# Kernel tuning notes

Hardware: AMD Instinct MI355X
Metric: run time of the kernel (lower is better)

## Reference

```python
import jax, jax.numpy as jnp
import numpy as np

B, GEO_CH, SEM_CH, H, W = 8, 256, 256, 64, 64
HS, WS = 32, 32  # semantic branch spatial size
EPS_ATTN = 1e-6
EPS_GN = 1e-5


def _phi(x):
    return jax.nn.elu(x) + 1.0


def setup_inputs() -> dict:
    key = jax.random.key(0)
    ks = jax.random.split(key, 8)
    f_geo = jax.random.normal(ks[0], (B, GEO_CH, H, W), dtype=jnp.float32)
    f_sem = jax.random.normal(ks[1], (B, SEM_CH, HS, WS), dtype=jnp.float32)
    s = 0.02
    Wq = jax.random.normal(ks[2], (SEM_CH, GEO_CH), dtype=jnp.float32) * s
    Wk = jax.random.normal(ks[3], (SEM_CH, SEM_CH), dtype=jnp.float32) * s
    Wv = jax.random.normal(ks[4], (SEM_CH, SEM_CH), dtype=jnp.float32) * s
    Wo = jax.random.normal(ks[5], (GEO_CH, SEM_CH), dtype=jnp.float32) * s
    bq = jnp.zeros((SEM_CH,), jnp.float32)
    bk = jnp.zeros((SEM_CH,), jnp.float32)
    bv = jnp.zeros((SEM_CH,), jnp.float32)
    bo = jnp.zeros((GEO_CH,), jnp.float32)
    gn_w = jnp.ones((GEO_CH,), jnp.float32)
    gn_b = jnp.zeros((GEO_CH,), jnp.float32)
    return {"f_geo": f_geo, "f_sem": f_sem, "Wq": Wq, "bq": bq, "Wk": Wk,
            "bk": bk, "Wv": Wv, "bv": bv, "Wo": Wo, "bo": bo,
            "gn_w": gn_w, "gn_b": gn_b}


def _conv1x1(x, Wm, b):
    # x: [B,Cin,H,W], Wm: [Cout,Cin] -> [B,Cout,H,W]
    return jnp.einsum('oc,bchw->bohw', Wm, x) + b[None, :, None, None]


def reference(f_geo, f_sem, Wq, bq, Wk, bk, Wv, bv, Wo, bo, gn_w, gn_b):
    b, cg, h, w = f_geo.shape
    n = h * w
    # bilinear resize, half-pixel centers == torch align_corners=False
    f_sem_r = jax.image.resize(f_sem, (b, f_sem.shape[1], h, w), method='bilinear')
    Q = _phi(_conv1x1(f_geo, Wq, bq)).reshape(b, -1, n)      # [B,Cs,N]
    K = _phi(_conv1x1(f_sem_r, Wk, bk)).reshape(b, -1, n)    # [B,Cs,N]
    V = _conv1x1(f_sem_r, Wv, bv).reshape(b, -1, n)          # [B,Cs,N]
    KV = jnp.einsum('bcn,bdn->bcd', K, V)                    # [B,Cs,Cs]
    QKV = jnp.einsum('bcn,bcd->bnd', Q, KV)                  # [B,N,Cs]
    K_sum = K.sum(axis=-1)                                   # [B,Cs]
    norm = jnp.einsum('bcn,bc->bn', Q, K_sum)[..., None] + EPS_ATTN  # [B,N,1]
    out = (QKV / norm).transpose(0, 2, 1).reshape(b, -1, h, w)
    y = f_geo + _conv1x1(out, Wo, bo)
    # GroupNorm(1, geo_ch): normalize over (C,H,W) per sample, per-channel affine
    mu = y.mean(axis=(1, 2, 3), keepdims=True)
    var = y.var(axis=(1, 2, 3), keepdims=True)
    yn = (y - mu) * jax.lax.rsqrt(var + EPS_GN)
    return yn * gn_w[None, :, None, None] + gn_b[None, :, None, None]
```

## Files before the change

kernel.cpp:

```cpp
#include <hip/hip_runtime.h>
#include <hip/hip_bf16.h>


#define B_ 8
#define C_ 256
#define H_ 64
#define W_ 64
#define N_ 4096
#define NS_ 1024
#define PIT 40
#define LDSZ (4 * 128 * PIT)
#define KVCH 16

typedef unsigned short u16;
using bf16x8 = __attribute__((ext_vector_type(8))) short;
using f32x4 = __attribute__((ext_vector_type(4))) float;

__device__ inline u16 f2bf(float f) {
  unsigned u = __builtin_bit_cast(unsigned, f);
  unsigned r = (u + 0x7fffu + ((u >> 16) & 1u)) >> 16;
  return (u16)r;
}
__device__ inline float bf2f(u16 x) {
  return __builtin_bit_cast(float, ((unsigned)x) << 16);
}

__device__ inline void gemm128_nt(const u16* __restrict__ At, const u16* __restrict__ Bt,
                                  int lda, int ldb, int k0, int k1,
                                  u16* __restrict__ lds, f32x4 acc[4][4])
{
  const int t = threadIdx.x;
  const int lane = t & 63;
  const int wave = t >> 6;
  const int wr = wave >> 1, wc = wave & 1;
  const int lr = lane & 15, lg = lane >> 4;
  const int sr = t >> 2, skv = t & 3;
  const size_t aoff = (size_t)sr * lda + skv * 8;
  const size_t aoff2 = (size_t)(sr + 64) * lda + skv * 8;
  const size_t boff = (size_t)sr * ldb + skv * 8;
  const size_t boff2 = (size_t)(sr + 64) * ldb + skv * 8;
  const int woff = sr * PIT + skv * 8;
  u16* A0 = lds;
  u16* B0 = lds + 128 * PIT;
  u16* A1 = lds + 2 * 128 * PIT;
  u16* B1 = lds + 3 * 128 * PIT;

  {
    uint4 a0 = *reinterpret_cast<const uint4*>(&At[aoff + k0]);
    uint4 a1 = *reinterpret_cast<const uint4*>(&At[aoff2 + k0]);
    uint4 b0 = *reinterpret_cast<const uint4*>(&Bt[boff + k0]);
    uint4 b1 = *reinterpret_cast<const uint4*>(&Bt[boff2 + k0]);
    *reinterpret_cast<uint4*>(&A0[woff]) = a0;
    *reinterpret_cast<uint4*>(&A0[woff + 64 * PIT]) = a1;
    *reinterpret_cast<uint4*>(&B0[woff]) = b0;
    *reinterpret_cast<uint4*>(&B0[woff + 64 * PIT]) = b1;
  }
  __syncthreads();
  int cur = 0;
  for (int k = k0; k < k1; k += 32) {
    uint4 na0, na1, nb0, nb1;
    const bool more = (k + 32) < k1;
    if (more) {
      na0 = *reinterpret_cast<const uint4*>(&At[aoff + k + 32]);
      na1 = *reinterpret_cast<const uint4*>(&At[aoff2 + k + 32]);
      nb0 = *reinterpret_cast<const uint4*>(&Bt[boff + k + 32]);
      nb1 = *reinterpret_cast<const uint4*>(&Bt[boff2 + k + 32]);
    }
    const u16* Ar = cur ? A1 : A0;
    const u16* Br = cur ? B1 : B0;
    const u16* ab = &Ar[(wr * 64 + lr) * PIT + lg * 8];
    const u16* bb = &Br[(wc * 64 + lr) * PIT + lg * 8];
    bf16x8 af[4], bfr[4];
#pragma unroll
    for (int i = 0; i < 4; ++i) af[i] = *reinterpret_cast<const bf16x8*>(ab + i * 16 * PIT);
#pragma unroll
    for (int i = 0; i < 4; ++i) bfr[i] = *reinterpret_cast<const bf16x8*>(bb + i * 16 * PIT);
#pragma unroll
    for (int m = 0; m < 4; ++m)
#pragma unroll
      for (int n = 0; n < 4; ++n)
        acc[m][n] = __builtin_amdgcn_mfma_f32_16x16x32_bf16(af[m], bfr[n], acc[m][n], 0, 0, 0);
    if (more) {
      u16* Aw = cur ? A0 : A1;
      u16* Bw = cur ? B0 : B1;
      *reinterpret_cast<uint4*>(&Aw[woff]) = na0;
      *reinterpret_cast<uint4*>(&Aw[woff + 64 * PIT]) = na1;
      *reinterpret_cast<uint4*>(&Bw[woff]) = nb0;
      *reinterpret_cast<uint4*>(&Bw[woff + 64 * PIT]) = nb1;
    }
    __syncthreads();
    cur ^= 1;
  }
}

__device__ inline void zero_acc(f32x4 acc[4][4]) {
#pragma unroll
  for (int m = 0; m < 4; ++m)
#pragma unroll
    for (int n = 0; n < 4; ++n)
#pragma unroll
      for (int r = 0; r < 4; ++r) acc[m][n][r] = 0.f;
}

__global__ __launch_bounds__(256) void k_transpose_cast(const float* __restrict__ in,
                                                        u16* __restrict__ out, int rows, int cols)
{
  __shared__ float tile[32][33];
  int b = blockIdx.z;
  const float* src = in + (size_t)b * rows * cols;
  u16* dst = out + (size_t)b * rows * cols;
  int c0 = blockIdx.x * 32, r0 = blockIdx.y * 32;
  int tx = threadIdx.x & 31, ty = threadIdx.x >> 5;
#pragma unroll
  for (int i = 0; i < 32; i += 8)
    tile[ty + i][tx] = src[(size_t)(r0 + ty + i) * cols + (c0 + tx)];
  __syncthreads();
#pragma unroll
  for (int i = 0; i < 32; i += 8)
    dst[(size_t)(c0 + ty + i) * rows + (r0 + tx)] = f2bf(tile[tx][ty + i]);
}

__global__ __launch_bounds__(256) void k_cast4(const float* __restrict__ w0, const float* __restrict__ w1,
                                               const float* __restrict__ w2, const float* __restrict__ w3,
                                               u16* o0, u16* o1, u16* o2, u16* o3,
                                               float* __restrict__ stats, float* __restrict__ normv)
{
  int i = blockIdx.x * 256 + threadIdx.x;
  o0[i] = f2bf(w0[i]); o1[i] = f2bf(w1[i]); o2[i] = f2bf(w2[i]); o3[i] = f2bf(w3[i]);
  if (i < 16) stats[i] = 0.f;
  if (i < B_ * N_) normv[i] = 1e-6f;
}

__global__ __launch_bounds__(256) void k_semconv(const u16* __restrict__ fsemT,
                                                 const u16* __restrict__ Wk, const u16* __restrict__ Wv,
                                                 const float* __restrict__ bk, const float* __restrict__ bv,
                                                 u16* __restrict__ Kpre, u16* __restrict__ Vpre)
{
  __shared__ u16 lds[LDSZ];
  int b = blockIdx.z >> 1, sel = blockIdx.z & 1;
  int m0 = blockIdx.y * 128, n0 = blockIdx.x * 128;
  const u16* A = (sel ? Wv : Wk) + (size_t)m0 * C_;
  const u16* Bm = fsemT + (size_t)b * NS_ * C_ + (size_t)n0 * C_;
  const float* bias = sel ? bv : bk;
  u16* out = (sel ? Vpre : Kpre) + (size_t)b * C_ * NS_;
  f32x4 acc[4][4];
  zero_acc(acc);
  gemm128_nt(A, Bm, C_, C_, 0, C_, lds, acc);
  int lane = threadIdx.x & 63, wave = threadIdx.x >> 6;
  int wr = wave >> 1, wc = wave & 1, lr = lane & 15, lg = lane >> 4;
#pragma unroll
  for (int m = 0; m < 4; ++m)
#pragma unroll
    for (int r = 0; r < 4; ++r) {
      int row = m0 + wr * 64 + m * 16 + lg * 4 + r;
      float bi = bias[row];
#pragma unroll
      for (int n = 0; n < 4; ++n) {
        int col = n0 + wc * 64 + n * 16 + lr;
        out[(size_t)row * NS_ + col] = f2bf(acc[m][n][r] + bi);
      }
    }
}

__global__ __launch_bounds__(256) void k_resize(const u16* __restrict__ Kpre, const u16* __restrict__ Vpre,
                                                u16* __restrict__ Kbf, u16* __restrict__ Vbf,
                                                float* __restrict__ Ksum)
{
  int sel = blockIdx.y;
  const u16* src = (sel ? Vpre : Kpre) + (size_t)blockIdx.x * NS_;
  u16* dst = (sel ? Vbf : Kbf) + (size_t)blockIdx.x * N_;
  float s = 0.f;
  for (int i = threadIdx.x; i < N_; i += 256) {
    int yy = i >> 6, xx = i & 63;
    int yh = yy >> 1, xh = xx >> 1;
    int ys0, ys1, xs0, xs1; float wy0, wy1, wx0, wx1;
    if (yy & 1) { ys0 = yh; ys1 = yh < 31 ? yh + 1 : 31; wy0 = 0.75f; wy1 = 0.25f; }
    else        { ys0 = yh > 0 ? yh - 1 : 0; ys1 = yh;   wy0 = 0.25f; wy1 = 0.75f; }
    if (xx & 1) { xs0 = xh; xs1 = xh < 31 ? xh + 1 : 31; wx0 = 0.75f; wx1 = 0.25f; }
    else        { xs0 = xh > 0 ? xh - 1 : 0; xs1 = xh;   wx0 = 0.25f; wx1 = 0.75f; }
    float r0 = wx0 * bf2f(src[ys0 * 32 + xs0]) + wx1 * bf2f(src[ys0 * 32 + xs1]);
    float r1 = wx0 * bf2f(src[ys1 * 32 + xs0]) + wx1 * bf2f(src[ys1 * 32 + xs1]);
    float v = wy0 * r0 + wy1 * r1;
    if (!sel) { v = v > 0.f ? v + 1.f : __expf(v); s += v; }
    dst[i] = f2bf(v);
  }
  if (!sel) {
    __shared__ float red[256];
    red[threadIdx.x] = s; __syncthreads();
    for (int off = 128; off > 0; off >>= 1) {
      if (threadIdx.x < off) red[threadIdx.x] += red[threadIdx.x + off];
      __syncthreads();
    }
    if (threadIdx.x == 0) Ksum[blockIdx.x] = red[0];
  }
}

__global__ __launch_bounds__(256) void k_kv(const u16* __restrict__ Kbf, const u16* __restrict__ Vbf,
                                            float* __restrict__ KVpart)
{
  __shared__ u16 lds[LDSZ];
  int tn = blockIdx.x, tm = blockIdx.y;
  int b = blockIdx.z >> 4, ch = blockIdx.z & 15;
  const int kspan = N_ / KVCH;
  const u16* A = Kbf + (size_t)b * C_ * N_ + (size_t)tm * 128 * N_;
  const u16* Bm = Vbf + (size_t)b * C_ * N_ + (size_t)tn * 128 * N_;
  f32x4 acc[4][4];
  zero_acc(acc);
  gemm128_nt(A, Bm, N_, N_, ch * kspan, ch * kspan + kspan, lds, acc);
  float* out = KVpart + ((size_t)(b * KVCH + ch) * 4 + tm * 2 + tn) * (128 * 128);
  int lane = threadIdx.x & 63, wave = threadIdx.x >> 6;
  int wr = wave >> 1, wc = wave & 1, lr = lane & 15, lg = lane >> 4;
#pragma unroll
  for (int m = 0; m < 4; ++m)
#pragma unroll
    for (int r = 0; r < 4; ++r)
#pragma unroll
      for (int n = 0; n < 4; ++n)
        out[(size_t)(wr * 64 + m * 16 + lg * 4 + r) * 128 + wc * 64 + n * 16 + lr] = acc[m][n][r];
}

__global__ __launch_bounds__(256) void k_kvred(const float* __restrict__ KVpart, u16* __restrict__ KVbf)
{
  int idx = blockIdx.x * 256 + threadIdx.x;
  int b = idx >> 16, cd = idx & 65535;
  int c = cd >> 8, d = cd & 255;
  int tile = (c >> 7) * 2 + (d >> 7);
  int loc = (c & 127) * 128 + (d & 127);
  float s = 0.f;
#pragma unroll
  for (int ch = 0; ch < KVCH; ++ch)
    s += KVpart[((size_t)(b * KVCH + ch) * 4 + tile) * 16384 + loc];
  KVbf[idx] = f2bf(s);
}

__global__ __launch_bounds__(256) void k_mgemm(const u16* __restrict__ Wo, const u16* __restrict__ KVbf,
                                               u16* __restrict__ Mbf)
{
  __shared__ u16 lds[LDSZ];
  int tn = blockIdx.x, tm = blockIdx.y, b = blockIdx.z;
  const u16* A = Wo + (size_t)tm * 128 * C_;
  const u16* Bm = KVbf + (size_t)b * C_ * C_ + (size_t)tn * 128 * C_;
  f32x4 acc[4][4];
  zero_acc(acc);
  gemm128_nt(A, Bm, C_, C_, 0, C_, lds, acc);
  u16* out = Mbf + (size_t)b * C_ * C_;
  int lane = threadIdx.x & 63, wave = threadIdx.x >> 6;
  int wr = wave >> 1, wc = wave & 1, lr = lane & 15, lg = lane >> 4;
#pragma unroll
  for (int m = 0; m < 4; ++m)
#pragma unroll
    for (int r = 0; r < 4; ++r)
#pragma unroll
      for (int n = 0; n < 4; ++n)
        out[(size_t)(tm * 128 + wr * 64 + m * 16 + lg * 4 + r) * C_ +
            tn * 128 + wc * 64 + n * 16 + lr] = f2bf(acc[m][n][r]);
}

__global__ __launch_bounds__(256) void k_qgemm(const u16* __restrict__ fgeoT, const u16* __restrict__ Wq,
                                               const float* __restrict__ bq, const float* __restrict__ Ksum,
                                               u16* __restrict__ Qt, float* __restrict__ normv)
{
  __shared__ u16 lds[LDSZ];
  int tc = blockIdx.x, tn = blockIdx.y, b = blockIdx.z;
  const u16* A = fgeoT + (size_t)b * N_ * C_ + (size_t)tn * 128 * C_;
  const u16* Bm = Wq + (size_t)tc * 128 * C_;
  f32x4 acc[4][4];
  zero_acc(acc);
  gemm128_nt(A, Bm, C_, C_, 0, C_, lds, acc);
  u16* out = Qt + (size_t)b * N_ * C_;
  int lane = threadIdx.x & 63, wave = threadIdx.x >> 6;
  int wr = wave >> 1, wc = wave & 1, lr = lane & 15, lg = lane >> 4;
  float bqv[4], ksv[4];
#pragma unroll
  for (int n = 0; n < 4; ++n) {
    int c = tc * 128 + wc * 64 + n * 16 + lr;
    bqv[n] = bq[c];
    ksv[n] = Ksum[b * C_ + c];
  }
  float pn[4][4];
#pragma unroll
  for (int m = 0; m < 4; ++m)
#pragma unroll
    for (int r = 0; r < 4; ++r) {
      int row = tn * 128 + wr * 64 + m * 16 + lg * 4 + r;
      float p = 0.f;
#pragma unroll
      for (int n = 0; n < 4; ++n) {
        float v = acc[m][n][r] + bqv[n];
        v = v > 0.f ? v + 1.f : __expf(v);
        out[(size_t)row * C_ + tc * 128 + wc * 64 + n * 16 + lr] = f2bf(v);
        p += v * ksv[n];
      }
      pn[m][r] = p;
    }
#pragma unroll
  for (int m = 0; m < 4; ++m)
#pragma unroll
    for (int r = 0; r < 4; ++r) {
      float p = pn[m][r];
      p += __shfl_xor(p, 1); p += __shfl_xor(p, 2);
      p += __shfl_xor(p, 4); p += __shfl_xor(p, 8);
      pn[m][r] = p;
    }
  if (lr == 0) {
    float* nb = normv + (size_t)b * N_;
#pragma unroll
    for (int m = 0; m < 4; ++m)
#pragma unroll
      for (int r = 0; r < 4; ++r) {
        int row = tn * 128 + wr * 64 + m * 16 + lg * 4 + r;
        atomicAdd(&nb[row], pn[m][r]);
      }
  }
}

__global__ __launch_bounds__(256) void k_final(const u16* __restrict__ Mbf, const u16* __restrict__ Qt,
                                               const float* __restrict__ fgeo, const float* __restrict__ bo,
                                               const float* __restrict__ normv,
                                               float* __restrict__ y, float* __restrict__ stats)
{
  __shared__ u16 lds[LDSZ];
  int tn = blockIdx.x, tm = blockIdx.y, b = blockIdx.z;
  const u16* A = Mbf + (size_t)b * C_ * C_ + (size_t)tm * 128 * C_;
  const u16* Bm = Qt + (size_t)b * N_ * C_ + (size_t)tn * 128 * C_;
  f32x4 acc[4][4];
  zero_acc(acc);
  gemm128_nt(A, Bm, C_, C_, 0, C_, lds, acc);
  int lane = threadIdx.x & 63, wave = threadIdx.x >> 6;
  int wr = wave >> 1, wc = wave & 1, lr = lane & 15, lg = lane >> 4;
  int m0 = tm * 128, n0 = tn * 128;
  const float* nrm = normv + (size_t)b * N_;
  float nv[4];
#pragma unroll
  for (int n = 0; n < 4; ++n) nv[n] = nrm[n0 + wc * 64 + n * 16 + lr];
  const float* fg = fgeo + (size_t)b * C_ * N_;
  float* yb = y + (size_t)b * C_ * N_;
  float ssum = 0.f, ssq = 0.f;
#pragma unroll
  for (int m = 0; m < 4; ++m)
#pragma unroll
    for (int r = 0; r < 4; ++r) {
      int row = m0 + wr * 64 + m * 16 + lg * 4 + r;
      float bov = bo[row];
#pragma unroll
      for (int n = 0; n < 4; ++n) {
        int col = n0 + wc * 64 + n * 16 + lr;
        float val = fg[(size_t)row * N_ + col] + bov + acc[m][n][r] / nv[n];
        yb[(size_t)row * N_ + col] = val;
        ssum += val; ssq += val * val;
      }
    }
#pragma unroll
  for (int off = 1; off < 64; off <<= 1) {
    ssum += __shfl_xor(ssum, off);
    ssq += __shfl_xor(ssq, off);
  }
  if (lane == 0) {
    atomicAdd(&stats[b * 2], ssum);
    atomicAdd(&stats[b * 2 + 1], ssq);
  }
}

__global__ __launch_bounds__(256) void k_gn(float* __restrict__ y, const float* __restrict__ stats,
                                            const float* __restrict__ gnw, const float* __restrict__ gnb)
{
  int idx = blockIdx.x * 256 + threadIdx.x;
  int elem = idx * 8;
  int b = elem >> 20;
  int o = (elem >> 12) & 255;
  const float cnt = (float)C_ * (float)N_;
  float mu = stats[b * 2] / cnt;
  float var = stats[b * 2 + 1] / cnt - mu * mu;
  float rs = rsqrtf(var + 1e-5f);
  float sc = gnw[o] * rs;
  float sh = gnb[o] - mu * sc;
  float4* p = reinterpret_cast<float4*>(y) + idx * 2;
  float4 v0 = p[0], v1 = p[1];
  v0.x = v0.x * sc + sh; v0.y = v0.y * sc + sh; v0.z = v0.z * sc + sh; v0.w = v0.w * sc + sh;
  v1.x = v1.x * sc + sh; v1.y = v1.y * sc + sh; v1.z = v1.z * sc + sh; v1.w = v1.w * sc + sh;
  p[0] = v0; p[1] = v1;
}

extern "C" void kernel_launch(void* const* d_in, const int* in_sizes, int n_in,
                              void* d_out, int out_size, void* d_ws, size_t ws_size,
                              hipStream_t stream)
{
  const float* f_geo = (const float*)d_in[0];
  const float* f_sem = (const float*)d_in[1];
  const float* Wq = (const float*)d_in[2];
  const float* bq = (const float*)d_in[3];
  const float* Wk = (const float*)d_in[4];
  const float* bk = (const float*)d_in[5];
  const float* Wv = (const float*)d_in[6];
  const float* bv = (const float*)d_in[7];
  const float* Wo = (const float*)d_in[8];
  const float* bo = (const float*)d_in[9];
  const float* gnw = (const float*)d_in[10];
  const float* gnb = (const float*)d_in[11];
  float* y = (float*)d_out;

  char* w = (char*)d_ws;
  auto alloc = [&](size_t bytes) { char* p = w; w += (bytes + 255) & ~(size_t)255; return p; };
  u16* fsemT = (u16*)alloc((size_t)B_ * NS_ * C_ * 2);
  u16* fgeoT = (u16*)alloc((size_t)B_ * N_ * C_ * 2);
  u16* Wqb = (u16*)alloc(65536 * 2);
  u16* Wkb = (u16*)alloc(65536 * 2);
  u16* Wvb = (u16*)alloc(65536 * 2);
  u16* Wob = (u16*)alloc(65536 * 2);
  u16* Kpre = (u16*)alloc((size_t)B_ * C_ * NS_ * 2);
  u16* Vpre = (u16*)alloc((size_t)B_ * C_ * NS_ * 2);
  u16* Kbf = (u16*)alloc((size_t)B_ * C_ * N_ * 2);
  u16* Vbf = (u16*)alloc((size_t)B_ * C_ * N_ * 2);
  float* Ksum = (float*)alloc((size_t)B_ * C_ * 4);
  float* KVpart = (float*)alloc((size_t)B_ * KVCH * 4 * 16384 * 4);
  u16* KVbf = (u16*)alloc((size_t)B_ * C_ * C_ * 2);
  u16* Mbf = (u16*)alloc((size_t)B_ * C_ * C_ * 2);
  u16* Qt = (u16*)alloc((size_t)B_ * N_ * C_ * 2);
  float* normv = (float*)alloc((size_t)B_ * N_ * 4);
  float* stats = (float*)alloc(256);

  k_transpose_cast<<<dim3(NS_ / 32, C_ / 32, B_), 256, 0, stream>>>(f_sem, fsemT, C_, NS_);
  k_transpose_cast<<<dim3(N_ / 32, C_ / 32, B_), 256, 0, stream>>>(f_geo, fgeoT, C_, N_);
  k_cast4<<<dim3(256), 256, 0, stream>>>(Wq, Wk, Wv, Wo, Wqb, Wkb, Wvb, Wob, stats, normv);
  k_semconv<<<dim3(8, 2, 16), 256, 0, stream>>>(fsemT, Wkb, Wvb, bk, bv, Kpre, Vpre);
  k_resize<<<dim3(B_ * C_, 2), 256, 0, stream>>>(Kpre, Vpre, Kbf, Vbf, Ksum);
  k_kv<<<dim3(2, 2, B_ * KVCH), 256, 0, stream>>>(Kbf, Vbf, KVpart);
  k_kvred<<<dim3(2048), 256, 0, stream>>>(KVpart, KVbf);
  k_mgemm<<<dim3(2, 2, B_), 256, 0, stream>>>(Wob, KVbf, Mbf);
  k_qgemm<<<dim3(2, 32, B_), 256, 0, stream>>>(fgeoT, Wqb, bq, Ksum, Qt, normv);
  k_final<<<dim3(32, 2, B_), 256, 0, stream>>>(Mbf, Qt, f_geo, bo, normv, y, stats);
  k_gn<<<dim3(B_ * C_ * N_ / 8 / 256), 256, 0, stream>>>(y, stats, gnw, gnb);
}
```

Measured before the change: 270.1 us.

## Use direct global-to-LDS loads in GEMM and stage epilogues through LDS

The shared GEMM mainloop now uses global_load_lds to copy tiles straight into unpadded LDS, dropping the register round-trip and the software double buffer. It relies on two barriers per k-step instead. All GEMM epilogues stage accumulators through an LDS buffer in two halves so each thread writes coalesced float4/ushort4 rows, and the q-GEMM norm reduction is reorganized around that. The risks are LDS bank conflicts from the unpadded 32-wide layout and less overlap of loads with MFMA work now that there is no prefetch.

```diff
diff --git a/kernel.cpp b/kernel.cpp
--- a/kernel.cpp
+++ b/kernel.cpp
@@ -4,12 +4,8 @@
 
 #define B_ 8
 #define C_ 256
-#define H_ 64
-#define W_ 64
 #define N_ 4096
 #define NS_ 1024
-#define PIT 40
-#define LDSZ (4 * 128 * PIT)
 #define KVCH 16
 
 typedef unsigned short u16;
@@ -25,71 +21,49 @@
   return __builtin_bit_cast(float, ((unsigned)x) << 16);
 }
 
+__device__ __forceinline__ void gl_lds16(const u16* g, u16* l) {
+  __builtin_amdgcn_global_load_lds((const __attribute__((address_space(1))) void*)g,
+                                   (__attribute__((address_space(3))) void*)l, 16, 0, 0);
+}
+
 __device__ inline void gemm128_nt(const u16* __restrict__ At, const u16* __restrict__ Bt,
                                   int lda, int ldb, int k0, int k1,
                                   u16* __restrict__ lds, f32x4 acc[4][4])
 {
   const int t = threadIdx.x;
-  const int lane = t & 63;
-  const int wave = t >> 6;
+  const int lane = t & 63, wave = t >> 6;
   const int wr = wave >> 1, wc = wave & 1;
   const int lr = lane & 15, lg = lane >> 4;
-  const int sr = t >> 2, skv = t & 3;
-  const size_t aoff = (size_t)sr * lda + skv * 8;
-  const size_t aoff2 = (size_t)(sr + 64) * lda + skv * 8;
-  const size_t boff = (size_t)sr * ldb + skv * 8;
-  const size_t boff2 = (size_t)(sr + 64) * ldb + skv * 8;
-  const int woff = sr * PIT + skv * 8;
-  u16* A0 = lds;
-  u16* B0 = lds + 128 * PIT;
-  u16* A1 = lds + 2 * 128 * PIT;
-  u16* B1 = lds + 3 * 128 * PIT;
-
-  {
-    uint4 a0 = *reinterpret_cast<const uint4*>(&At[aoff + k0]);
-    uint4 a1 = *reinterpret_cast<const uint4*>(&At[aoff2 + k0]);
-    uint4 b0 = *reinterpret_cast<const uint4*>(&Bt[boff + k0]);
-    uint4 b1 = *reinterpret_cast<const uint4*>(&Bt[boff2 + k0]);
-    *reinterpret_cast<uint4*>(&A0[woff]) = a0;
-    *reinterpret_cast<uint4*>(&A0[woff + 64 * PIT]) = a1;
-    *reinterpret_cast<uint4*>(&B0[woff]) = b0;
-    *reinterpret_cast<uint4*>(&B0[woff + 64 * PIT]) = b1;
-  }
-  __syncthreads();
-  int cur = 0;
+  const int sr = t >> 2, skv = (t & 3) * 8;
+  u16* Ab = lds;
+  u16* Bb = lds + 128 * 32;
+  const u16* gA0 = At + (size_t)sr * lda + skv;
+  const u16* gA1 = At + (size_t)(sr + 64) * lda + skv;
+  const u16* gB0 = Bt + (size_t)sr * ldb + skv;
+  const u16* gB1 = Bt + (size_t)(sr + 64) * ldb + skv;
+  u16* dA0 = Ab + wave * 512;
+  u16* dA1 = Ab + 2048 + wave * 512;
+  u16* dB0 = Bb + wave * 512;
+  u16* dB1 = Bb + 2048 + wave * 512;
+  const u16* ap = Ab + (wr * 64 + lr) * 32 + lg * 8;
+  const u16* bp = Bb + (wc * 64 + lr) * 32 + lg * 8;
   for (int k = k0; k < k1; k += 32) {
-    uint4 na0, na1, nb0, nb1;
-    const bool more = (k + 32) < k1;
-    if (more) {
-      na0 = *reinterpret_cast<const uint4*>(&At[aoff + k + 32]);
-      na1 = *reinterpret_cast<const uint4*>(&At[aoff2 + k + 32]);
-      nb0 = *reinterpret_cast<const uint4*>(&Bt[boff + k + 32]);
-      nb1 = *reinterpret_cast<const uint4*>(&Bt[boff2 + k + 32]);
-    }
-    const u16* Ar = cur ? A1 : A0;
-    const u16* Br = cur ? B1 : B0;
-    const u16* ab = &Ar[(wr * 64 + lr) * PIT + lg * 8];
-    const u16* bb = &Br[(wc * 64 + lr) * PIT + lg * 8];
+    gl_lds16(gA0 + k, dA0);
+    gl_lds16(gA1 + k, dA1);
+    gl_lds16(gB0 + k, dB0);
+    gl_lds16(gB1 + k, dB1);
+    __syncthreads();
     bf16x8 af[4], bfr[4];
 #pragma unroll
-    for (int i = 0; i < 4; ++i) af[i] = *reinterpret_cast<const bf16x8*>(ab + i * 16 * PIT);
-#pragma unroll
-    for (int i = 0; i < 4; ++i) bfr[i] = *reinterpret_cast<const bf16x8*>(bb + i * 16 * PIT);
+    for (int i = 0; i < 4; ++i) af[i] = *reinterpret_cast<const bf16x8*>(ap + i * 16 * 32);
+#pragma unroll
+    for (int i = 0; i < 4; ++i) bfr[i] = *reinterpret_cast<const bf16x8*>(bp + i * 16 * 32);
 #pragma unroll
     for (int m = 0; m < 4; ++m)
 #pragma unroll
       for (int n = 0; n < 4; ++n)
         acc[m][n] = __builtin_amdgcn_mfma_f32_16x16x32_bf16(af[m], bfr[n], acc[m][n], 0, 0, 0);
-    if (more) {
-      u16* Aw = cur ? A0 : A1;
-      u16* Bw = cur ? B0 : B1;
-      *reinterpret_cast<uint4*>(&Aw[woff]) = na0;
-      *reinterpret_cast<uint4*>(&Aw[woff + 64 * PIT]) = na1;
-      *reinterpret_cast<uint4*>(&Bw[woff]) = nb0;
-      *reinterpret_cast<uint4*>(&Bw[woff + 64 * PIT]) = nb1;
-    }
-    __syncthreads();
-    cur ^= 1;
+    __syncthreads();
   }
 }
 
@@ -100,6 +74,20 @@
     for (int n = 0; n < 4; ++n)
 #pragma unroll
       for (int r = 0; r < 4; ++r) acc[m][n][r] = 0.f;
+}
+
+__device__ inline void ep_stage_half(const f32x4 acc[4][4], float* eplds, int h,
+                                     int wr, int wc, int lr, int lg)
+{
+  if (wr == h) {
+#pragma unroll
+    for (int m = 0; m < 4; ++m)
+#pragma unroll
+      for (int n = 0; n < 4; ++n)
+#pragma unroll
+        for (int r = 0; r < 4; ++r)
+          eplds[(m * 16 + lg * 4 + r) * 132 + wc * 64 + n * 16 + lr] = acc[m][n][r];
+  }
 }
 
 __global__ __launch_bounds__(256) void k_transpose_cast(const float* __restrict__ in,
@@ -136,7 +124,8 @@
                                                  const float* __restrict__ bk, const float* __restrict__ bv,
                                                  u16* __restrict__ Kpre, u16* __restrict__ Vpre)
 {
-  __shared__ u16 lds[LDSZ];
+  __shared__ u16 glds[2 * 128 * 32];
+  __shared__ float eplds[64 * 132];
   int b = blockIdx.z >> 1, sel = blockIdx.z & 1;
   int m0 = blockIdx.y * 128, n0 = blockIdx.x * 128;
   const u16* A = (sel ? Wv : Wk) + (size_t)m0 * C_;
@@ -145,21 +134,24 @@
   u16* out = (sel ? Vpre : Kpre) + (size_t)b * C_ * NS_;
   f32x4 acc[4][4];
   zero_acc(acc);
-  gemm128_nt(A, Bm, C_, C_, 0, C_, lds, acc);
-  int lane = threadIdx.x & 63, wave = threadIdx.x >> 6;
+  gemm128_nt(A, Bm, C_, C_, 0, C_, glds, acc);
+  int t = threadIdx.x, lane = t & 63, wave = t >> 6;
   int wr = wave >> 1, wc = wave & 1, lr = lane & 15, lg = lane >> 4;
-#pragma unroll
-  for (int m = 0; m < 4; ++m)
-#pragma unroll
-    for (int r = 0; r < 4; ++r) {
-      int row = m0 + wr * 64 + m * 16 + lg * 4 + r;
+  for (int h = 0; h < 2; ++h) {
+    __syncthreads();
+    ep_stage_half(acc, eplds, h, wr, wc, lr, lg);
+    __syncthreads();
+#pragma unroll
+    for (int it = 0; it < 8; ++it) {
+      int rloc = it * 8 + (t >> 5), cloc = (t & 31) * 4;
+      int row = m0 + h * 64 + rloc;
+      float4 a = *(const float4*)&eplds[rloc * 132 + cloc];
       float bi = bias[row];
-#pragma unroll
-      for (int n = 0; n < 4; ++n) {
-        int col = n0 + wc * 64 + n * 16 + lr;
-        out[(size_t)row * NS_ + col] = f2bf(acc[m][n][r] + bi);
-      }
-    }
+      ushort4 o;
+      o.x = f2bf(a.x + bi); o.y = f2bf(a.y + bi); o.z = f2bf(a.z + bi); o.w = f2bf(a.w + bi);
+      *(ushort4*)&out[(size_t)row * NS_ + n0 + cloc] = o;
+    }
+  }
 }
 
 __global__ __launch_bounds__(256) void k_resize(const u16* __restrict__ Kpre, const u16* __restrict__ Vpre,
@@ -198,7 +190,8 @@
 __global__ __launch_bounds__(256) void k_kv(const u16* __restrict__ Kbf, const u16* __restrict__ Vbf,
                                             float* __restrict__ KVpart)
 {
-  __shared__ u16 lds[LDSZ];
+  __shared__ u16 glds[2 * 128 * 32];
+  __shared__ float eplds[64 * 132];
   int tn = blockIdx.x, tm = blockIdx.y;
   int b = blockIdx.z >> 4, ch = blockIdx.z & 15;
   const int kspan = N_ / KVCH;
@@ -206,17 +199,21 @@
   const u16* Bm = Vbf + (size_t)b * C_ * N_ + (size_t)tn * 128 * N_;
   f32x4 acc[4][4];
   zero_acc(acc);
-  gemm128_nt(A, Bm, N_, N_, ch * kspan, ch * kspan + kspan, lds, acc);
+  gemm128_nt(A, Bm, N_, N_, ch * kspan, ch * kspan + kspan, glds, acc);
   float* out = KVpart + ((size_t)(b * KVCH + ch) * 4 + tm * 2 + tn) * (128 * 128);
-  int lane = threadIdx.x & 63, wave = threadIdx.x >> 6;
+  int t = threadIdx.x, lane = t & 63, wave = t >> 6;
   int wr = wave >> 1, wc = wave & 1, lr = lane & 15, lg = lane >> 4;
-#pragma unroll
-  for (int m = 0; m < 4; ++m)
-#pragma unroll
-    for (int r = 0; r < 4; ++r)
-#pragma unroll
-      for (int n = 0; n < 4; ++n)
-        out[(size_t)(wr * 64 + m * 16 + lg * 4 + r) * 128 + wc * 64 + n * 16 + lr] = acc[m][n][r];
+  for (int h = 0; h < 2; ++h) {
+    __syncthreads();
+    ep_stage_half(acc, eplds, h, wr, wc, lr, lg);
+    __syncthreads();
+#pragma unroll
+    for (int it = 0; it < 8; ++it) {
+      int rloc = it * 8 + (t >> 5), cloc = (t & 31) * 4;
+      float4 a = *(const float4*)&eplds[rloc * 132 + cloc];
+      *(float4*)&out[(size_t)(h * 64 + rloc) * 128 + cloc] = a;
+    }
+  }
 }
 
 __global__ __launch_bounds__(256) void k_kvred(const float* __restrict__ KVpart, u16* __restrict__ KVbf)
@@ -236,81 +233,73 @@
 __global__ __launch_bounds__(256) void k_mgemm(const u16* __restrict__ Wo, const u16* __restrict__ KVbf,
                                                u16* __restrict__ Mbf)
 {
-  __shared__ u16 lds[LDSZ];
+  __shared__ u16 glds[2 * 128 * 32];
+  __shared__ float eplds[64 * 132];
   int tn = blockIdx.x, tm = blockIdx.y, b = blockIdx.z;
   const u16* A = Wo + (size_t)tm * 128 * C_;
   const u16* Bm = KVbf + (size_t)b * C_ * C_ + (size_t)tn * 128 * C_;
   f32x4 acc[4][4];
   zero_acc(acc);
-  gemm128_nt(A, Bm, C_, C_, 0, C_, lds, acc);
+  gemm128_nt(A, Bm, C_, C_, 0, C_, glds, acc);
   u16* out = Mbf + (size_t)b * C_ * C_;
-  int lane = threadIdx.x & 63, wave = threadIdx.x >> 6;
+  int t = threadIdx.x, lane = t & 63, wave = t >> 6;
   int wr = wave >> 1, wc = wave & 1, lr = lane & 15, lg = lane >> 4;
-#pragma unroll
-  for (int m = 0; m < 4; ++m)
-#pragma unroll
-    for (int r = 0; r < 4; ++r)
-#pragma unroll
-      for (int n = 0; n < 4; ++n)
-        out[(size_t)(tm * 128 + wr * 64 + m * 16 + lg * 4 + r) * C_ +
-            tn * 128 + wc * 64 + n * 16 + lr] = f2bf(acc[m][n][r]);
+  for (int h = 0; h < 2; ++h) {
+    __syncthreads();
+    ep_stage_half(acc, eplds, h, wr, wc, lr, lg);
+    __syncthreads();
+#pragma unroll
+    for (int it = 0; it < 8; ++it) {
+      int rloc = it * 8 + (t >> 5), cloc = (t & 31) * 4;
+      int row = tm * 128 + h * 64 + rloc;
+      float4 a = *(const float4*)&eplds[rloc * 132 + cloc];
+      ushort4 o;
+      o.x = f2bf(a.x); o.y = f2bf(a.y); o.z = f2bf(a.z); o.w = f2bf(a.w);
+      *(ushort4*)&out[(size_t)row * C_ + tn * 128 + cloc] = o;
+    }
+  }
 }
 
 __global__ __launch_bounds__(256) void k_qgemm(const u16* __restrict__ fgeoT, const u16* __restrict__ Wq,
                                                const float* __restrict__ bq, const float* __restrict__ Ksum,
                                                u16* __restrict__ Qt, float* __restrict__ normv)
 {
-  __shared__ u16 lds[LDSZ];
+  __shared__ u16 glds[2 * 128 * 32];
+  __shared__ float eplds[64 * 132];
   int tc = blockIdx.x, tn = blockIdx.y, b = blockIdx.z;
   const u16* A = fgeoT + (size_t)b * N_ * C_ + (size_t)tn * 128 * C_;
   const u16* Bm = Wq + (size_t)tc * 128 * C_;
   f32x4 acc[4][4];
   zero_acc(acc);
-  gemm128_nt(A, Bm, C_, C_, 0, C_, lds, acc);
+  gemm128_nt(A, Bm, C_, C_, 0, C_, glds, acc);
   u16* out = Qt + (size_t)b * N_ * C_;
-  int lane = threadIdx.x & 63, wave = threadIdx.x >> 6;
+  float* nb = normv + (size_t)b * N_;
+  int t = threadIdx.x, lane = t & 63, wave = t >> 6;
   int wr = wave >> 1, wc = wave & 1, lr = lane & 15, lg = lane >> 4;
-  float bqv[4], ksv[4];
-#pragma unroll
-  for (int n = 0; n < 4; ++n) {
-    int c = tc * 128 + wc * 64 + n * 16 + lr;
-    bqv[n] = bq[c];
-    ksv[n] = Ksum[b * C_ + c];
-  }
-  float pn[4][4];
-#pragma unroll
-  for (int m = 0; m < 4; ++m)
-#pragma unroll
-    for (int r = 0; r < 4; ++r) {
-      int row = tn * 128 + wr * 64 + m * 16 + lg * 4 + r;
-      float p = 0.f;
-#pragma unroll
-      for (int n = 0; n < 4; ++n) {
-        float v = acc[m][n][r] + bqv[n];
-        v = v > 0.f ? v + 1.f : __expf(v);
-        out[(size_t)row * C_ + tc * 128 + wc * 64 + n * 16 + lr] = f2bf(v);
-        p += v * ksv[n];
-      }
-      pn[m][r] = p;
-    }
-#pragma unroll
-  for (int m = 0; m < 4; ++m)
-#pragma unroll
-    for (int r = 0; r < 4; ++r) {
-      float p = pn[m][r];
+  for (int h = 0; h < 2; ++h) {
+    __syncthreads();
+    ep_stage_half(acc, eplds, h, wr, wc, lr, lg);
+    __syncthreads();
+#pragma unroll
+    for (int it = 0; it < 8; ++it) {
+      int rloc = it * 8 + (t >> 5), cloc = (t & 31) * 4;
+      int row = tn * 128 + h * 64 + rloc;
+      int col = tc * 128 + cloc;
+      float4 a = *(const float4*)&eplds[rloc * 132 + cloc];
+      float4 bqv = *(const float4*)&bq[col];
+      float4 ks = *(const float4*)&Ksum[b * C_ + col];
+      float v0 = a.x + bqv.x; v0 = v0 > 0.f ? v0 + 1.f : __expf(v0);
+      float v1 = a.y + bqv.y; v1 = v1 > 0.f ? v1 + 1.f : __expf(v1);
+      float v2 = a.z + bqv.z; v2 = v2 > 0.f ? v2 + 1.f : __expf(v2);
+      float v3 = a.w + bqv.w; v3 = v3 > 0.f ? v3 + 1.f : __expf(v3);
+      ushort4 o;
+      o.x = f2bf(v0); o.y = f2bf(v1); o.z = f2bf(v2); o.w = f2bf(v3);
+      *(ushort4*)&out[(size_t)row * C_ + col] = o;
+      float p = v0 * ks.x + v1 * ks.y + v2 * ks.z + v3 * ks.w;
       p += __shfl_xor(p, 1); p += __shfl_xor(p, 2);
-      p += __shfl_xor(p, 4); p += __shfl_xor(p, 8);
-      pn[m][r] = p;
-    }
-  if (lr == 0) {
-    float* nb = normv + (size_t)b * N_;
-#pragma unroll
-    for (int m = 0; m < 4; ++m)
-#pragma unroll
-      for (int r = 0; r < 4; ++r) {
-        int row = tn * 128 + wr * 64 + m * 16 + lg * 4 + r;
-        atomicAdd(&nb[row], pn[m][r]);
-      }
+      p += __shfl_xor(p, 4); p += __shfl_xor(p, 8); p += __shfl_xor(p, 16);
+      if ((t & 31) == 0) atomicAdd(&nb[row], p);
+    }
   }
 }
 
@@ -319,37 +308,43 @@
                                                const float* __restrict__ normv,
                                                float* __restrict__ y, float* __restrict__ stats)
 {
-  __shared__ u16 lds[LDSZ];
+  __shared__ u16 glds[2 * 128 * 32];
+  __shared__ float eplds[64 * 132];
   int tn = blockIdx.x, tm = blockIdx.y, b = blockIdx.z;
   const u16* A = Mbf + (size_t)b * C_ * C_ + (size_t)tm * 128 * C_;
   const u16* Bm = Qt + (size_t)b * N_ * C_ + (size_t)tn * 128 * C_;
   f32x4 acc[4][4];
   zero_acc(acc);
-  gemm128_nt(A, Bm, C_, C_, 0, C_, lds, acc);
-  int lane = threadIdx.x & 63, wave = threadIdx.x >> 6;
-  int wr = wave >> 1, wc = wave & 1, lr = lane & 15, lg = lane >> 4;
-  int m0 = tm * 128, n0 = tn * 128;
+  gemm128_nt(A, Bm, C_, C_, 0, C_, glds, acc);
   const float* nrm = normv + (size_t)b * N_;
-  float nv[4];
-#pragma unroll
-  for (int n = 0; n < 4; ++n) nv[n] = nrm[n0 + wc * 64 + n * 16 + lr];
   const float* fg = fgeo + (size_t)b * C_ * N_;
   float* yb = y + (size_t)b * C_ * N_;
+  int t = threadIdx.x, lane = t & 63, wave = t >> 6;
+  int wr = wave >> 1, wc = wave & 1, lr = lane & 15, lg = lane >> 4;
   float ssum = 0.f, ssq = 0.f;
-#pragma unroll
-  for (int m = 0; m < 4; ++m)
-#pragma unroll
-    for (int r = 0; r < 4; ++r) {
-      int row = m0 + wr * 64 + m * 16 + lg * 4 + r;
+  for (int h = 0; h < 2; ++h) {
+    __syncthreads();
+    ep_stage_half(acc, eplds, h, wr, wc, lr, lg);
+    __syncthreads();
+#pragma unroll
+    for (int it = 0; it < 8; ++it) {
+      int rloc = it * 8 + (t >> 5), cloc = (t & 31) * 4;
+      int row = tm * 128 + h * 64 + rloc;
+      int col = tn * 128 + cloc;
+      float4 a = *(const float4*)&eplds[rloc * 132 + cloc];
+      float4 nv = *(const float4*)&nrm[col];
+      float4 f = *(const float4*)&fg[(size_t)row * N_ + col];
       float bov = bo[row];
-#pragma unroll
-      for (int n = 0; n < 4; ++n) {
-        int col = n0 + wc * 64 + n * 16 + lr;
-        float val = fg[(size_t)row * N_ + col] + bov + acc[m][n][r] / nv[n];
-        yb[(size_t)row * N_ + col] = val;
-        ssum += val; ssq += val * val;
-      }
-    }
+      float4 v;
+      v.x = f.x + bov + a.x / nv.x;
+      v.y = f.y + bov + a.y / nv.y;
+      v.z = f.z + bov + a.z / nv.z;
+      v.w = f.w + bov + a.w / nv.w;
+      *(float4*)&yb[(size_t)row * N_ + col] = v;
+      ssum += v.x + v.y + v.z + v.w;
+      ssq += v.x * v.x + v.y * v.y + v.z * v.z + v.w * v.w;
+    }
+  }
 #pragma unroll
   for (int off = 1; off < 64; off <<= 1) {
     ssum += __shfl_xor(ssum, off);
```

Result: no change. 266.1 us (-1.5%).
